# Kernel optimization log

Hardware: AMD Instinct MI355X
Metric: run time of the kernel (lower is better)

Reference implementation:

```python
import jax, jax.numpy as jnp
import numpy as np

# DAG: node -> list of children; node 0 is the stem output, node 6 is the cell output.
GRAPH = {1: [0], 2: [0, 1], 3: [1, 2], 4: [2, 3], 5: [3, 4], 6: [4, 5]}
OUTPUT_NODE = 6


def conv3x3(x, w, b):
    # x: [N,C,H,W], w: [O,I,3,3], b: [O]; stride 1, SAME padding (PyTorch Conv2d pad=1)
    y = jax.lax.conv_general_dilated(
        x, w, window_strides=(1, 1), padding='SAME',
        dimension_numbers=('NCHW', 'OIHW', 'NCHW'))
    return y + b[None, :, None, None]


def setup_inputs() -> dict:
    key = jax.random.key(0)
    k_x, k_w0, k_b0, k_wn, k_bn = jax.random.split(key, 5)
    scale = 0.05  # keep activations bounded through 7 stacked convs
    return {
        'x': jax.random.normal(k_x, (8, 64, 64, 64), dtype=jnp.float32),
        'W0': jax.random.normal(k_w0, (128, 64, 3, 3), dtype=jnp.float32) * scale,
        'b0': jax.random.normal(k_b0, (128,), dtype=jnp.float32) * scale,
        'Wn': jax.random.normal(k_wn, (6, 128, 128, 3, 3), dtype=jnp.float32) * scale,
        'bn': jax.random.normal(k_bn, (6, 128), dtype=jnp.float32) * scale,
    }


def reference(x, W0, b0, Wn, bn):
    # activations[0] = layers['0'](x)
    acts = {0: conv3x3(x, W0, b0)}
    # DFS with memoization over a DAG == topological evaluation of nodes 1..6.
    # Each node n sums its OWN conv (weights Wn[n-1]) applied to every child activation.
    for node in range(1, OUTPUT_NODE + 1):
        w, b = Wn[node - 1], bn[node - 1]
        out = None
        for child in GRAPH[node]:
            y = conv3x3(acts[child], w, b)
            out = y if out is None else out + y
        acts[node] = out
    return acts[OUTPUT_NODE]
```

## Files before the change

kernel.cpp:

```cpp
#include <hip/hip_runtime.h>


typedef __bf16 bf16x8 __attribute__((ext_vector_type(8)));
typedef float f32x4 __attribute__((ext_vector_type(4)));

union U4 { uint4 u; bf16x8 b; };

__device__ inline unsigned pk_bf16(float lo, float hi) {
  unsigned r;
  asm volatile("v_cvt_pk_bf16_f32 %0, %1, %2" : "=v"(r) : "v"(lo), "v"(hi));
  return r;
}

__device__ inline unsigned addpk(unsigned a, unsigned b) {
  float alo = __builtin_bit_cast(float, a << 16);
  float ahi = __builtin_bit_cast(float, a & 0xFFFF0000u);
  float blo = __builtin_bit_cast(float, b << 16);
  float bhi = __builtin_bit_cast(float, b & 0xFFFF0000u);
  return pk_bf16(alo + blo, ahi + bhi);
}

__device__ inline uint4 addpk4(uint4 a, uint4 b) {
  return make_uint4(addpk(a.x, b.x), addpk(a.y, b.y), addpk(a.z, b.z), addpk(a.w, b.w));
}

__device__ __forceinline__ void gload16(const unsigned* g, unsigned* l) {
  __builtin_amdgcn_global_load_lds(
      (const __attribute__((address_space(1))) unsigned*)(g),
      (__attribute__((address_space(3))) unsigned*)(l), 16, 0, 0);
}

template <int N>
__device__ __forceinline__ void waitcnt_vm_lgkm() {
  if constexpr (N == 0)
    asm volatile("s_waitcnt vmcnt(0) lgkmcnt(0)" ::: "memory");
  else if constexpr (N == 1)
    asm volatile("s_waitcnt vmcnt(1) lgkmcnt(0)" ::: "memory");
  else
    asm volatile("s_waitcnt vmcnt(2) lgkmcnt(0)" ::: "memory");
}

__device__ __forceinline__ void seal_lgkm_barrier() {
  asm volatile("s_waitcnt lgkmcnt(0)" ::: "memory");
  __builtin_amdgcn_s_barrier();
  __builtin_amdgcn_sched_barrier(0);
}

#define WB_WORDS 479232

__global__ __launch_bounds__(512) void setup_all(
    const float* __restrict__ x, const float* __restrict__ W0,
    const float* __restrict__ Wn, unsigned* __restrict__ B0,
    unsigned* __restrict__ B1, unsigned* __restrict__ B2,
    unsigned* __restrict__ T, unsigned* __restrict__ Wb) {
  __shared__ float xl[2 * 64 * 65];
  const int tid = threadIdx.x;
  const int bid = blockIdx.x;
  const int n = bid & 7;

#pragma unroll
  for (int it = 0; it < 4; ++it) {
    unsigned gid = (unsigned)bid * 512 + tid + it * 131072u;
    if (gid < WB_WORDS) {
      const float* src;
      int CIN, c, r, j;
      if (gid < 36864) {
        src = W0; CIN = 64;
        c = gid >> 11; int w = gid & 2047; r = w >> 5; j = w & 31;
      } else {
        unsigned g2 = gid - 36864;
        int s = g2 / 73728; unsigned r2 = g2 % 73728;
        src = Wn + (size_t)s * 147456; CIN = 128;
        c = r2 >> 12; int w = r2 & 4095; r = w >> 6; j = w & 63;
      }
      int ochalf = c / 9, tap = c % 9;
      int dy = tap / 3, dx = tap % 3;
      int icpair = j ^ ((r & 7) << 2);
      int oc = ochalf * 64 + r;
      size_t base = (((size_t)oc * CIN + 2 * icpair) * 3 + dy) * 3 + dx;
      Wb[gid] = pk_bf16(src[base], src[base + 9]);
    }
  }

  {
    unsigned gid = (unsigned)bid * 512 + tid;
    if (gid < 116480) {
      unsigned* buf; int CW; unsigned u;
      if (gid < 99840) {
        buf = gid < 33280 ? B0 : (gid < 66560 ? B1 : B2);
        u = gid % 33280; CW = 64;
      } else {
        buf = T; u = gid - 99840; CW = 32;
      }
      int per_n = 65 * CW;
      int nn = u / per_n;
      unsigned v = u % per_n;
      int pix = (v * 4) / CW, cw = (v * 4) % CW;
      int row, col;
      if (pix < 66) { row = 0; col = pix; }
      else if (pix < 132) { row = 65; col = pix - 66; }
      else if (pix < 196) { row = pix - 131; col = 0; }
      else { row = pix - 195; col = 65; }
      *(uint4*)&buf[((((size_t)nn * 66 + row) * 66 + col) * CW) + cw] =
          make_uint4(0, 0, 0, 0);
    }
  }

  {
    int hh = bid >> 3;
    int sub = tid >> 8;
    int t8 = tid & 255;
    int h = hh * 2 + sub;
#pragma unroll
    for (int k = 0; k < 16; ++k) {
      int idx = t8 + k * 256;
      int ic = idx >> 6, w = idx & 63;
      xl[(sub * 64 + w) * 65 + ic] = x[(((size_t)n * 64 + ic) * 64 + h) * 64 + w];
    }
    __syncthreads();
#pragma unroll
    for (int k = 0; k < 8; ++k) {
      int idx = t8 + k * 256;
      int w = idx >> 5, icp = idx & 31;
      unsigned v = pk_bf16(xl[(sub * 64 + w) * 65 + icp * 2],
                           xl[(sub * 64 + w) * 65 + icp * 2 + 1]);
      int wp = w + 1;
      int pos = icp ^ ((wp & 7) << 2);
      T[(((size_t)n * 66 + (h + 1)) * 66 + wp) * 32 + pos] = v;
    }
  }
}

__global__ __launch_bounds__(512, 2) void conv_stem(
    const unsigned* __restrict__ in0, const unsigned* __restrict__ wb,
    const float* __restrict__ bias, unsigned* __restrict__ outp) {
  constexpr int WPP = 32, CHW = 2048, WL = 1, ROWW = 66 * 32;
  constexpr int ACTW = 6 * ROWW, ALDS_W = 16384;
  constexpr int R4_U4 = 4 * ROWW / 4, R2_U4 = 2 * ROWW / 4;
  constexpr int AJ4 = (R4_U4 + 511) / 512, LJ = (R2_U4 + 511) / 512;

  __shared__ unsigned Alds[ALDS_W];
  __shared__ unsigned Wlds[3][CHW];

  const int tid = threadIdx.x;
  const int lane = tid & 63;
  const int wav = tid >> 6;
  const int wr = wav >> 1;
  const int kh = wav & 1;
  const int l15 = lane & 15, q = lane >> 4;
  const int bid = blockIdx.x;
  const int n = bid & 7;
  const int ochalf = (bid >> 3) & 1;
  const int h0 = (bid >> 4) * 4;

  const unsigned* wbase = wb + (size_t)ochalf * 9 * CHW;
  const size_t abase = ((size_t)n * 66 + h0) * ROWW;
  const uint4* g0 = (const uint4*)(in0 + abase);

  uint4 l0[LJ];
#pragma unroll
  for (int j = 0; j < LJ; ++j) {
    int i = tid + j * 512;
    if (i < R2_U4) l0[j] = g0[R4_U4 + i];
  }
#pragma unroll
  for (int j = 0; j < AJ4; ++j) {
    int i = tid + j * 512;
    if (i < R4_U4) *(uint4*)&Alds[4 * i] = g0[i];
  }
#pragma unroll
  for (int s = 0; s < WL; ++s)
    gload16(wbase + s * 2048 + tid * 4, &Wlds[0][s * 2048 + wav * 256]);
#pragma unroll
  for (int s = 0; s < WL; ++s)
    gload16(wbase + CHW + s * 2048 + tid * 4, &Wlds[1][s * 2048 + wav * 256]);
  seal_lgkm_barrier();

  f32x4 acc[4][4];
#pragma unroll
  for (int m = 0; m < 4; ++m)
#pragma unroll
    for (int p = 0; p < 4; ++p) acc[m][p] = (f32x4)0.f;

#pragma unroll
  for (int t = 0; t < 9; ++t) {
    if (t < 8) waitcnt_vm_lgkm<WL>();
    else waitcnt_vm_lgkm<0>();
    __builtin_amdgcn_s_barrier();
    __builtin_amdgcn_sched_barrier(0);

    const unsigned* WB = Wlds[t % 3];
    const int dy = t / 3, dx = t % 3;
    const int arow = (wr + dy) * 66;
    const int kc = kh;

    __builtin_amdgcn_s_setprio(1);
    bf16x8 a[4];
#pragma unroll
    for (int m = 0; m < 4; ++m) {
      int r = m * 16 + l15;
      U4 u;
      u.u = *(const uint4*)&WB[r * WPP + ((kc * 16 + q * 4) ^ ((r & 7) << 2))];
      a[m] = u.b;
    }
#pragma unroll
    for (int p = 0; p < 4; ++p) {
      int col = p * 16 + l15 + dx;
      U4 u;
      u.u = *(const uint4*)&Alds[(arow + col) * WPP +
                                 ((kc * 16 + q * 4) ^ ((col & 7) << 2))];
      bf16x8 b = u.b;
#pragma unroll
      for (int m = 0; m < 4; ++m)
        acc[m][p] = __builtin_amdgcn_mfma_f32_16x16x32_bf16(a[m], b, acc[m][p], 0, 0, 0);
    }
    __builtin_amdgcn_s_setprio(0);
    __builtin_amdgcn_sched_barrier(0);

    if (t == 0) {
#pragma unroll
      for (int j = 0; j < LJ; ++j) {
        int i = tid + j * 512;
        if (i < R2_U4) *(uint4*)&Alds[4 * (R4_U4 + i)] = l0[j];
      }
    }
    if (t + 2 < 9) {
#pragma unroll
      for (int s = 0; s < WL; ++s)
        gload16(wbase + (size_t)(t + 2) * CHW + s * 2048 + tid * 4,
                &Wlds[(t + 2) % 3][s * 2048 + wav * 256]);
    }
    __builtin_amdgcn_sched_barrier(0);
  }

  __syncthreads();
  float* R = (float*)Alds;
  if (kh) {
#pragma unroll
    for (int m = 0; m < 4; ++m)
#pragma unroll
      for (int p = 0; p < 4; ++p)
        *(f32x4*)&R[(wr * 16 + m * 4 + p) * 256 + lane * 4] = acc[m][p];
  }
  __syncthreads();
  if (kh) return;
#pragma unroll
  for (int m = 0; m < 4; ++m)
#pragma unroll
    for (int p = 0; p < 4; ++p)
      acc[m][p] += *(const f32x4*)&R[(wr * 16 + m * 4 + p) * 256 + lane * 4];

  const int obase = ochalf * 64;
#pragma unroll
  for (int m = 0; m < 4; ++m) {
    int oc0 = obase + m * 16 + q * 4;
    float4 bb = *(const float4*)&bias[oc0];
    int icp0 = oc0 >> 1;
#pragma unroll
    for (int p = 0; p < 4; ++p) {
      int w = p * 16 + l15;
      int wp = w + 1;
      unsigned lo = pk_bf16(acc[m][p][0] + bb.x, acc[m][p][1] + bb.y);
      unsigned hi = pk_bf16(acc[m][p][2] + bb.z, acc[m][p][3] + bb.w);
      int pos = icp0 ^ ((wp & 7) << 2);
      size_t base = (((size_t)n * 66 + (h0 + 1 + wr)) * 66 + wp) * 64;
      *(uint2*)&outp[base + pos] = make_uint2(lo, hi);
    }
  }
}

template <bool DUAL, bool OUTF32>
__global__ __launch_bounds__(512, 2) void conv_node(
    const unsigned* __restrict__ in0, const unsigned* __restrict__ in1,
    const unsigned* __restrict__ wb, const float* __restrict__ bias,
    float bmult, void* __restrict__ outp) {
  constexpr int WPP = 64, CHW = 4096, WL = 2, ROWW = 66 * 64;
  constexpr int ACTW = 6 * ROWW;
  constexpr int R4_U4 = 4 * ROWW / 4, R2_U4 = 2 * ROWW / 4;
  constexpr int AJ4 = (R4_U4 + 511) / 512, LJ = (R2_U4 + 511) / 512;

  __shared__ unsigned Alds[ACTW];
  __shared__ unsigned Wlds[3][CHW];

  const int tid = threadIdx.x;
  const int lane = tid & 63;
  const int wav = tid >> 6;
  const int wp = wav & 1;
  const int kh = wav >> 1;
  const int l15 = lane & 15, q = lane >> 4;
  const int bid = blockIdx.x;
  const int n = bid & 7;
  const int ochalf = (bid >> 3) & 1;
  const int h0 = (bid >> 4) * 4;

  const unsigned* wbase = wb + (size_t)ochalf * 9 * CHW;
  const size_t abase = ((size_t)n * 66 + h0) * ROWW;
  const uint4* g0 = (const uint4*)(in0 + abase);
  const uint4* g1 = (const uint4*)(in1 + abase);

  uint4 l0[LJ], l1[LJ];
#pragma unroll
  for (int j = 0; j < LJ; ++j) {
    int i = tid + j * 512;
    if (i < R2_U4) {
      l0[j] = g0[R4_U4 + i];
      if (DUAL) l1[j] = g1[R4_U4 + i];
    }
  }
#pragma unroll
  for (int j = 0; j < AJ4; ++j) {
    int i = tid + j * 512;
    if (i < R4_U4) {
      uint4 v = g0[i];
      if (DUAL) v = addpk4(v, g1[i]);
      *(uint4*)&Alds[4 * i] = v;
    }
  }
#pragma unroll
  for (int s = 0; s < WL; ++s)
    gload16(wbase + s * 2048 + tid * 4, &Wlds[0][s * 2048 + wav * 256]);
#pragma unroll
  for (int s = 0; s < WL; ++s)
    gload16(wbase + CHW + s * 2048 + tid * 4, &Wlds[1][s * 2048 + wav * 256]);
  seal_lgkm_barrier();

  f32x4 acc[4][8];
#pragma unroll
  for (int m = 0; m < 4; ++m)
#pragma unroll
    for (int p = 0; p < 8; ++p) acc[m][p] = (f32x4)0.f;

  const int kq = kh * 16 + q * 4;

#pragma unroll
  for (int t = 0; t < 9; ++t) {
    if (t < 8) waitcnt_vm_lgkm<WL>();
    else waitcnt_vm_lgkm<0>();
    __builtin_amdgcn_s_barrier();
    __builtin_amdgcn_sched_barrier(0);

    const unsigned* WB = Wlds[t % 3];
    const int dy = t / 3, dx = t % 3;

    __builtin_amdgcn_s_setprio(1);
    bf16x8 a[4];
#pragma unroll
    for (int m = 0; m < 4; ++m) {
      int r = m * 16 + l15;
      U4 u;
      u.u = *(const uint4*)&WB[r * WPP + (kq ^ ((r & 7) << 2))];
      a[m] = u.b;
    }
#pragma unroll
    for (int p = 0; p < 8; ++p) {
      int row_in = 2 * wp + (p >> 2) + dy;
      int col = (p & 3) * 16 + l15 + dx;
      U4 u;
      u.u = *(const uint4*)&Alds[(row_in * 66 + col) * WPP +
                                 (kq ^ ((col & 7) << 2))];
      bf16x8 b = u.b;
#pragma unroll
      for (int m = 0; m < 4; ++m)
        acc[m][p] = __builtin_amdgcn_mfma_f32_16x16x32_bf16(a[m], b, acc[m][p], 0, 0, 0);
    }
    __builtin_amdgcn_s_setprio(0);
    __builtin_amdgcn_sched_barrier(0);

    if (t == 0) {
#pragma unroll
      for (int j = 0; j < LJ; ++j) {
        int i = tid + j * 512;
        if (i < R2_U4) {
          uint4 v = l0[j];
          if (DUAL) v = addpk4(v, l1[j]);
          *(uint4*)&Alds[4 * (R4_U4 + i)] = v;
        }
      }
    }
    if (t + 2 < 9) {
#pragma unroll
      for (int s = 0; s < WL; ++s)
        gload16(wbase + (size_t)(t + 2) * CHW + s * 2048 + tid * 4,
                &Wlds[(t + 2) % 3][s * 2048 + wav * 256]);
    }
    __builtin_amdgcn_sched_barrier(0);
  }

  __syncthreads();
  if (kh != 0) {
    unsigned* Rb = &Alds[((kh - 1) * 2 + wp) * 4096];
#pragma unroll
    for (int m = 0; m < 4; ++m)
#pragma unroll
      for (int p = 0; p < 8; ++p) {
        unsigned u0 = pk_bf16(acc[m][p][0], acc[m][p][1]);
        unsigned u1 = pk_bf16(acc[m][p][2], acc[m][p][3]);
        *(uint2*)&Rb[(m * 8 + p) * 128 + lane * 2] = make_uint2(u0, u1);
      }
  }
  __syncthreads();
  if (kh != 0) return;

#pragma unroll
  for (int gi = 0; gi < 3; ++gi) {
    const unsigned* Rb = &Alds[(gi * 2 + wp) * 4096];
#pragma unroll
    for (int m = 0; m < 4; ++m)
#pragma unroll
      for (int p = 0; p < 8; ++p) {
        uint2 v = *(const uint2*)&Rb[(m * 8 + p) * 128 + lane * 2];
        acc[m][p][0] += __builtin_bit_cast(float, v.x << 16);
        acc[m][p][1] += __builtin_bit_cast(float, v.x & 0xFFFF0000u);
        acc[m][p][2] += __builtin_bit_cast(float, v.y << 16);
        acc[m][p][3] += __builtin_bit_cast(float, v.y & 0xFFFF0000u);
      }
  }

  const int obase = ochalf * 64;
  if (OUTF32) {
    float* out = (float*)outp;
#pragma unroll
    for (int m = 0; m < 4; ++m) {
      int oc0 = obase + m * 16 + q * 4;
      float4 bb = *(const float4*)&bias[oc0];
#pragma unroll
      for (int p = 0; p < 8; ++p) {
        int row = h0 + 2 * wp + (p >> 2);
        int wcol = (p & 3) * 16 + l15;
#pragma unroll
        for (int j = 0; j < 4; ++j)
          out[(((size_t)n * 128 + oc0 + j) * 64 + row) * 64 + wcol] =
              acc[m][p][j] + ((const float*)&bb)[j] * bmult;
      }
    }
  } else {
    unsigned* out = (unsigned*)outp;
#pragma unroll
    for (int m = 0; m < 4; ++m) {
      int oc0 = obase + m * 16 + q * 4;
      float4 bb = *(const float4*)&bias[oc0];
      int icp0 = oc0 >> 1;
#pragma unroll
      for (int p = 0; p < 8; ++p) {
        int row_out = h0 + 1 + 2 * wp + (p >> 2);
        int wpad = (p & 3) * 16 + l15 + 1;
        unsigned lo = pk_bf16(acc[m][p][0] + bb.x * bmult, acc[m][p][1] + bb.y * bmult);
        unsigned hi = pk_bf16(acc[m][p][2] + bb.z * bmult, acc[m][p][3] + bb.w * bmult);
        int pos = icp0 ^ ((wpad & 7) << 2);
        size_t base = (((size_t)n * 66 + row_out) * 66 + wpad) * 64;
        *(uint2*)&out[base + pos] = make_uint2(lo, hi);
      }
    }
  }
}

extern "C" void kernel_launch(void* const* d_in, const int* in_sizes, int n_in,
                              void* d_out, int out_size, void* d_ws,
                              size_t ws_size, hipStream_t stream) {
  const float* x = (const float*)d_in[0];
  const float* W0 = (const float*)d_in[1];
  const float* b0 = (const float*)d_in[2];
  const float* Wn = (const float*)d_in[3];
  const float* bn = (const float*)d_in[4];

  const size_t ACTB = (size_t)8 * 66 * 66 * 64;
  const size_t TW = (size_t)8 * 66 * 66 * 32;
  unsigned* B0 = (unsigned*)d_ws;
  unsigned* B1 = B0 + ACTB;
  unsigned* B2 = B1 + ACTB;
  unsigned* T = B2 + ACTB;
  unsigned* Wb = T + TW;

  setup_all<<<256, 512, 0, stream>>>(x, W0, Wn, B0, B1, B2, T, Wb);

  dim3 grid(256), blk(512);
  const unsigned* Wnode = Wb + 36864;
  const size_t NW = 73728;

  conv_stem<<<grid, blk, 0, stream>>>(T, Wb, b0, B0);
  conv_node<false, false><<<grid, blk, 0, stream>>>(B0, B0, Wnode, bn + 0, 1.f, B1);
  conv_node<true, false><<<grid, blk, 0, stream>>>(B0, B1, Wnode + 1 * NW, bn + 128, 2.f, B2);
  conv_node<true, false><<<grid, blk, 0, stream>>>(B1, B2, Wnode + 2 * NW, bn + 256, 2.f, B0);
  conv_node<true, false><<<grid, blk, 0, stream>>>(B2, B0, Wnode + 3 * NW, bn + 384, 2.f, B1);
  conv_node<true, false><<<grid, blk, 0, stream>>>(B0, B1, Wnode + 4 * NW, bn + 512, 2.f, B2);
  conv_node<true, true><<<grid, blk, 0, stream>>>(B1, B2, Wnode + 5 * NW, bn + 640, 2.f, d_out);

  (void)in_sizes; (void)n_in; (void)out_size; (void)ws_size;
}
```

Baseline: 125.6 us.

## Split node conv into 2-row tiles with K-halved channel staging

Each node-conv block now covers 2 output rows instead of 4 and uses 256 threads, so the grid grows from 256 to 512 blocks. Input channels are staged in two 64-channel halves (18 K-steps), with the second half prefetched into registers during the first. The weight layout is reordered so each tap-half chunk is contiguous, and the cross-wave K reduction now passes fp32 partials through LDS instead of bf16. The aim is more blocks with less LDS each for better occupancy and load balance, at the cost of more halo re-reads per output row and twice as many barriered steps.

After: 125.8 us. Within noise of the previous version (+0.1%).

```diff
diff --git a/kernel.cpp b/kernel.cpp
--- a/kernel.cpp
+++ b/kernel.cpp
@@ -62,23 +62,29 @@
   for (int it = 0; it < 4; ++it) {
     unsigned gid = (unsigned)bid * 512 + tid + it * 131072u;
     if (gid < WB_WORDS) {
-      const float* src;
-      int CIN, c, r, j;
+      unsigned val;
       if (gid < 36864) {
-        src = W0; CIN = 64;
-        c = gid >> 11; int w = gid & 2047; r = w >> 5; j = w & 31;
+        int c = gid >> 11; int w = gid & 2047; int r = w >> 5; int j = w & 31;
+        int ochalf = c / 9, tap = c % 9;
+        int dy = tap / 3, dx = tap % 3;
+        int icpair = j ^ ((r & 7) << 2);
+        int oc = ochalf * 64 + r;
+        size_t base = (((size_t)oc * 64 + 2 * icpair) * 3 + dy) * 3 + dx;
+        val = pk_bf16(W0[base], W0[base + 9]);
       } else {
         unsigned g2 = gid - 36864;
         int s = g2 / 73728; unsigned r2 = g2 % 73728;
-        src = Wn + (size_t)s * 147456; CIN = 128;
-        c = r2 >> 12; int w = r2 & 4095; r = w >> 6; j = w & 63;
-      }
-      int ochalf = c / 9, tap = c % 9;
-      int dy = tap / 3, dx = tap % 3;
-      int icpair = j ^ ((r & 7) << 2);
-      int oc = ochalf * 64 + r;
-      size_t base = (((size_t)oc * CIN + 2 * icpair) * 3 + dy) * 3 + dx;
-      Wb[gid] = pk_bf16(src[base], src[base + 9]);
+        const float* src = Wn + (size_t)s * 147456;
+        int c2 = r2 >> 11; int w = r2 & 2047; int r = w >> 5; int j = w & 31;
+        int och = c2 / 18; int rest = c2 % 18;
+        int khalf = rest / 9, tap = rest % 9;
+        int dy = tap / 3, dx = tap % 3;
+        int icp = khalf * 32 + (j ^ ((r & 7) << 2));
+        int oc = och * 64 + r;
+        size_t base = (((size_t)oc * 128 + 2 * icp) * 3 + dy) * 3 + dx;
+        val = pk_bf16(src[base], src[base + 9]);
+      }
+      Wb[gid] = val;
     }
   }
 
@@ -135,7 +141,7 @@
     const unsigned* __restrict__ in0, const unsigned* __restrict__ wb,
     const float* __restrict__ bias, unsigned* __restrict__ outp) {
   constexpr int WPP = 32, CHW = 2048, WL = 1, ROWW = 66 * 32;
-  constexpr int ACTW = 6 * ROWW, ALDS_W = 16384;
+  constexpr int ALDS_W = 16384;
   constexpr int R4_U4 = 4 * ROWW / 4, R2_U4 = 2 * ROWW / 4;
   constexpr int AJ4 = (R4_U4 + 511) / 512, LJ = (R2_U4 + 511) / 512;
 
@@ -270,77 +276,86 @@
 }
 
 template <bool DUAL, bool OUTF32>
-__global__ __launch_bounds__(512, 2) void conv_node(
+__global__ __launch_bounds__(256, 2) void conv_node(
     const unsigned* __restrict__ in0, const unsigned* __restrict__ in1,
     const unsigned* __restrict__ wb, const float* __restrict__ bias,
     float bmult, void* __restrict__ outp) {
-  constexpr int WPP = 64, CHW = 4096, WL = 2, ROWW = 66 * 64;
-  constexpr int ACTW = 6 * ROWW;
-  constexpr int R4_U4 = 4 * ROWW / 4, R2_U4 = 2 * ROWW / 4;
-  constexpr int AJ4 = (R4_U4 + 511) / 512, LJ = (R2_U4 + 511) / 512;
-
-  __shared__ unsigned Alds[ACTW];
+  constexpr int CHW = 2048;
+  constexpr int WL = 2;
+  constexpr int H_U4 = 2112;
+  constexpr int HJ = (H_U4 + 255) / 256;
+
+  __shared__ unsigned Alds[8448];
   __shared__ unsigned Wlds[3][CHW];
 
   const int tid = threadIdx.x;
   const int lane = tid & 63;
   const int wav = tid >> 6;
-  const int wp = wav & 1;
-  const int kh = wav >> 1;
+  const int wr = wav >> 1;
+  const int kh = wav & 1;
   const int l15 = lane & 15, q = lane >> 4;
   const int bid = blockIdx.x;
   const int n = bid & 7;
   const int ochalf = (bid >> 3) & 1;
-  const int h0 = (bid >> 4) * 4;
-
-  const unsigned* wbase = wb + (size_t)ochalf * 9 * CHW;
-  const size_t abase = ((size_t)n * 66 + h0) * ROWW;
+  const int hp = bid >> 4;
+  const int h0 = hp * 2;
+
+  const unsigned* wbase = wb + (size_t)ochalf * 18 * CHW;
+  const size_t abase = ((size_t)n * 66 + h0) * (66 * 64);
   const uint4* g0 = (const uint4*)(in0 + abase);
   const uint4* g1 = (const uint4*)(in1 + abase);
 
-  uint4 l0[LJ], l1[LJ];
-#pragma unroll
-  for (int j = 0; j < LJ; ++j) {
-    int i = tid + j * 512;
-    if (i < R2_U4) {
-      l0[j] = g0[R4_U4 + i];
-      if (DUAL) l1[j] = g1[R4_U4 + i];
-    }
-  }
-#pragma unroll
-  for (int j = 0; j < AJ4; ++j) {
-    int i = tid + j * 512;
-    if (i < R4_U4) {
-      uint4 v = g0[i];
-      if (DUAL) v = addpk4(v, g1[i]);
+#pragma unroll
+  for (int j = 0; j < HJ; ++j) {
+    int i = tid + j * 256;
+    if (i < H_U4) {
+      int gi = ((i >> 3) << 4) + (i & 7);
+      uint4 v = g0[gi];
+      if (DUAL) v = addpk4(v, g1[gi]);
       *(uint4*)&Alds[4 * i] = v;
     }
   }
 #pragma unroll
   for (int s = 0; s < WL; ++s)
-    gload16(wbase + s * 2048 + tid * 4, &Wlds[0][s * 2048 + wav * 256]);
+    gload16(wbase + s * 1024 + tid * 4, &Wlds[0][s * 1024 + wav * 256]);
 #pragma unroll
   for (int s = 0; s < WL; ++s)
-    gload16(wbase + CHW + s * 2048 + tid * 4, &Wlds[1][s * 2048 + wav * 256]);
+    gload16(wbase + CHW + s * 1024 + tid * 4, &Wlds[1][s * 1024 + wav * 256]);
   seal_lgkm_barrier();
 
-  f32x4 acc[4][8];
+  f32x4 acc[4][4];
 #pragma unroll
   for (int m = 0; m < 4; ++m)
 #pragma unroll
-    for (int p = 0; p < 8; ++p) acc[m][p] = (f32x4)0.f;
-
+    for (int p = 0; p < 4; ++p) acc[m][p] = (f32x4)0.f;
+
+  uint4 l0[HJ], l1[HJ];
   const int kq = kh * 16 + q * 4;
 
 #pragma unroll
-  for (int t = 0; t < 9; ++t) {
-    if (t < 8) waitcnt_vm_lgkm<WL>();
+  for (int t = 0; t < 18; ++t) {
+    if (t < 17) waitcnt_vm_lgkm<WL>();
     else waitcnt_vm_lgkm<0>();
     __builtin_amdgcn_s_barrier();
     __builtin_amdgcn_sched_barrier(0);
 
+    if (t == 9) {
+#pragma unroll
+      for (int j = 0; j < HJ; ++j) {
+        int i = tid + j * 256;
+        if (i < H_U4) {
+          uint4 v = l0[j];
+          if (DUAL) v = addpk4(v, l1[j]);
+          *(uint4*)&Alds[4 * i] = v;
+        }
+      }
+      seal_lgkm_barrier();
+    }
+
     const unsigned* WB = Wlds[t % 3];
-    const int dy = t / 3, dx = t % 3;
+    const int tap = t % 9;
+    const int dy = tap / 3, dx = tap % 3;
+    const int arow = (wr + dy) * 66;
 
     __builtin_amdgcn_s_setprio(1);
     bf16x8 a[4];
@@ -348,16 +363,14 @@
     for (int m = 0; m < 4; ++m) {
       int r = m * 16 + l15;
       U4 u;
-      u.u = *(const uint4*)&WB[r * WPP + (kq ^ ((r & 7) << 2))];
+      u.u = *(const uint4*)&WB[r * 32 + (kq ^ ((r & 7) << 2))];
       a[m] = u.b;
     }
 #pragma unroll
-    for (int p = 0; p < 8; ++p) {
-      int row_in = 2 * wp + (p >> 2) + dy;
-      int col = (p & 3) * 16 + l15 + dx;
+    for (int p = 0; p < 4; ++p) {
+      int col = p * 16 + l15 + dx;
       U4 u;
-      u.u = *(const uint4*)&Alds[(row_in * 66 + col) * WPP +
-                                 (kq ^ ((col & 7) << 2))];
+      u.u = *(const uint4*)&Alds[(arow + col) * 32 + (kq ^ ((col & 7) << 2))];
       bf16x8 b = u.b;
 #pragma unroll
       for (int m = 0; m < 4; ++m)
@@ -366,55 +379,42 @@
     __builtin_amdgcn_s_setprio(0);
     __builtin_amdgcn_sched_barrier(0);
 
-    if (t == 0) {
-#pragma unroll
-      for (int j = 0; j < LJ; ++j) {
-        int i = tid + j * 512;
-        if (i < R2_U4) {
-          uint4 v = l0[j];
-          if (DUAL) v = addpk4(v, l1[j]);
-          *(uint4*)&Alds[4 * (R4_U4 + i)] = v;
+    if (t == 8) {
+#pragma unroll
+      for (int j = 0; j < HJ; ++j) {
+        int i = tid + j * 256;
+        if (i < H_U4) {
+          int gi = ((i >> 3) << 4) + 8 + (i & 7);
+          l0[j] = g0[gi];
+          if (DUAL) l1[j] = g1[gi];
         }
       }
     }
-    if (t + 2 < 9) {
+    if (t + 2 < 18) {
 #pragma unroll
       for (int s = 0; s < WL; ++s)
-        gload16(wbase + (size_t)(t + 2) * CHW + s * 2048 + tid * 4,
-                &Wlds[(t + 2) % 3][s * 2048 + wav * 256]);
+        gload16(wbase + (size_t)(t + 2) * CHW + s * 1024 + tid * 4,
+                &Wlds[(t + 2) % 3][s * 1024 + wav * 256]);
     }
     __builtin_amdgcn_sched_barrier(0);
   }
 
   __syncthreads();
-  if (kh != 0) {
-    unsigned* Rb = &Alds[((kh - 1) * 2 + wp) * 4096];
+  float* R = (float*)Alds;
+  if (kh) {
 #pragma unroll
     for (int m = 0; m < 4; ++m)
 #pragma unroll
-      for (int p = 0; p < 8; ++p) {
-        unsigned u0 = pk_bf16(acc[m][p][0], acc[m][p][1]);
-        unsigned u1 = pk_bf16(acc[m][p][2], acc[m][p][3]);
-        *(uint2*)&Rb[(m * 8 + p) * 128 + lane * 2] = make_uint2(u0, u1);
-      }
+      for (int p = 0; p < 4; ++p)
+        *(f32x4*)&R[(wr * 16 + m * 4 + p) * 256 + lane * 4] = acc[m][p];
   }
   __syncthreads();
-  if (kh != 0) return;
-
-#pragma unroll
-  for (int gi = 0; gi < 3; ++gi) {
-    const unsigned* Rb = &Alds[(gi * 2 + wp) * 4096];
-#pragma unroll
-    for (int m = 0; m < 4; ++m)
-#pragma unroll
-      for (int p = 0; p < 8; ++p) {
-        uint2 v = *(const uint2*)&Rb[(m * 8 + p) * 128 + lane * 2];
-        acc[m][p][0] += __builtin_bit_cast(float, v.x << 16);
-        acc[m][p][1] += __builtin_bit_cast(float, v.x & 0xFFFF0000u);
-        acc[m][p][2] += __builtin_bit_cast(float, v.y << 16);
-        acc[m][p][3] += __builtin_bit_cast(float, v.y & 0xFFFF0000u);
-      }
-  }
+  if (kh) return;
+#pragma unroll
+  for (int m = 0; m < 4; ++m)
+#pragma unroll
+    for (int p = 0; p < 4; ++p)
+      acc[m][p] += *(const f32x4*)&R[(wr * 16 + m * 4 + p) * 256 + lane * 4];
 
   const int obase = ochalf * 64;
   if (OUTF32) {
@@ -424,12 +424,11 @@
       int oc0 = obase + m * 16 + q * 4;
       float4 bb = *(const float4*)&bias[oc0];
 #pragma unroll
-      for (int p = 0; p < 8; ++p) {
-        int row = h0 + 2 * wp + (p >> 2);
-        int wcol = (p & 3) * 16 + l15;
+      for (int p = 0; p < 4; ++p) {
+        int w = p * 16 + l15;
 #pragma unroll
         for (int j = 0; j < 4; ++j)
-          out[(((size_t)n * 128 + oc0 + j) * 64 + row) * 64 + wcol] =
+          out[(((size_t)n * 128 + oc0 + j) * 64 + (h0 + wr)) * 64 + w] =
               acc[m][p][j] + ((const float*)&bb)[j] * bmult;
       }
     }
@@ -441,13 +440,13 @@
       float4 bb = *(const float4*)&bias[oc0];
       int icp0 = oc0 >> 1;
 #pragma unroll
-      for (int p = 0; p < 8; ++p) {
-        int row_out = h0 + 1 + 2 * wp + (p >> 2);
-        int wpad = (p & 3) * 16 + l15 + 1;
+      for (int p = 0; p < 4; ++p) {
+        int w = p * 16 + l15;
+        int wp = w + 1;
         unsigned lo = pk_bf16(acc[m][p][0] + bb.x * bmult, acc[m][p][1] + bb.y * bmult);
         unsigned hi = pk_bf16(acc[m][p][2] + bb.z * bmult, acc[m][p][3] + bb.w * bmult);
-        int pos = icp0 ^ ((wpad & 7) << 2);
-        size_t base = (((size_t)n * 66 + row_out) * 66 + wpad) * 64;
+        int pos = icp0 ^ ((wp & 7) << 2);
+        size_t base = (((size_t)n * 66 + (h0 + 1 + wr)) * 66 + wp) * 64;
         *(uint2*)&out[base + pos] = make_uint2(lo, hi);
       }
     }
@@ -473,17 +472,16 @@
 
   setup_all<<<256, 512, 0, stream>>>(x, W0, Wn, B0, B1, B2, T, Wb);
 
-  dim3 grid(256), blk(512);
   const unsigned* Wnode = Wb + 36864;
   const size_t NW = 73728;
 
-  conv_stem<<<grid, blk, 0, stream>>>(T, Wb, b0, B0);
-  conv_node<false, false><<<grid, blk, 0, stream>>>(B0, B0, Wnode, bn + 0, 1.f, B1);
-  conv_node<true, false><<<grid, blk, 0, stream>>>(B0, B1, Wnode + 1 * NW, bn + 128, 2.f, B2);
-  conv_node<true, false><<<grid, blk, 0, stream>>>(B1, B2, Wnode + 2 * NW, bn + 256, 2.f, B0);
-  conv_node<true, false><<<grid, blk, 0, stream>>>(B2, B0, Wnode + 3 * NW, bn + 384, 2.f, B1);
-  conv_node<true, false><<<grid, blk, 0, stream>>>(B0, B1, Wnode + 4 * NW, bn + 512, 2.f, B2);
-  conv_node<true, true><<<grid, blk, 0, stream>>>(B1, B2, Wnode + 5 * NW, bn + 640, 2.f, d_out);
+  conv_stem<<<256, 512, 0, stream>>>(T, Wb, b0, B0);
+  conv_node<false, false><<<512, 256, 0, stream>>>(B0, B0, Wnode, bn + 0, 1.f, B1);
+  conv_node<true, false><<<512, 256, 0, stream>>>(B0, B1, Wnode + 1 * NW, bn + 128, 2.f, B2);
+  conv_node<true, false><<<512, 256, 0, stream>>>(B1, B2, Wnode + 2 * NW, bn + 256, 2.f, B0);
+  conv_node<true, false><<<512, 256, 0, stream>>>(B2, B0, Wnode + 3 * NW, bn + 384, 2.f, B1);
+  conv_node<true, false><<<512, 256, 0, stream>>>(B0, B1, Wnode + 4 * NW, bn + 512, 2.f, B2);
+  conv_node<true, true><<<512, 256, 0, stream>>>(B1, B2, Wnode + 5 * NW, bn + 640, 2.f, d_out);
 
   (void)in_sizes; (void)n_in; (void)out_size; (void)ws_size;
 }
```
